# Kernel tuning notes

Hardware: AMD Instinct MI355X
Metric: run time of the kernel (lower is better)

The kernel has to match this reference:

```python
import jax, jax.numpy as jnp
import numpy as np

N = 4096          # num_nodes
D_MODEL = 256     # embedding_dim
H = 8             # num_heads
DH = D_MODEL // H # dim_head = 32
E_RAND = N * 32   # random edges (avg degree 32)


def setup_inputs() -> dict:
    key = jax.random.key(0)
    ks = jax.random.split(key, 12)
    s = 0.02
    x = jax.random.normal(ks[0], (N, D_MODEL), jnp.float32)
    src = jax.random.randint(ks[1], (E_RAND,), 0, N)
    dst = jax.random.randint(ks[2], (E_RAND,), 0, N)
    loops = jnp.arange(N)
    # add self-loops so no softmax row is all -inf
    edge_index = jnp.stack([jnp.concatenate([src, loops]),
                            jnp.concatenate([dst, loops])]).astype(jnp.int64)
    Wq = jax.random.normal(ks[3], (D_MODEL, D_MODEL), jnp.float32) * s
    bq = jnp.zeros((D_MODEL,), jnp.float32)
    Wk = jax.random.normal(ks[4], (D_MODEL, D_MODEL), jnp.float32) * s
    bk = jnp.zeros((D_MODEL,), jnp.float32)
    Wv = jax.random.normal(ks[5], (D_MODEL, D_MODEL), jnp.float32) * s
    bv = jnp.zeros((D_MODEL,), jnp.float32)
    Wp = jax.random.normal(ks[6], (D_MODEL, 2 * D_MODEL), jnp.float32) * s
    bp = jnp.zeros((D_MODEL,), jnp.float32)
    return {"x": x, "edge_index": edge_index,
            "Wq": Wq, "bq": bq, "Wk": Wk, "bk": bk,
            "Wv": Wv, "bv": bv, "Wp": Wp, "bp": bp}


def reference(x, edge_index, Wq, bq, Wk, bk, Wv, bv, Wp, bp):
    n = x.shape[0]
    # projections -> [H, N, DH]
    q = (x @ Wq.T + bq).reshape(n, H, DH).transpose(1, 0, 2)
    k = (x @ Wk.T + bk).reshape(n, H, DH).transpose(1, 0, 2)
    v = (x @ Wv.T + bv).reshape(n, H, DH).transpose(1, 0, 2)
    scale = 1.0 / jnp.sqrt(jnp.asarray(DH, x.dtype))
    att = jnp.einsum('hnd,hmd->hnm', q, k) * scale   # [H, N, N]
    # original: mask = ones(N,N); mask[e0,e1]=False; masked_fill(mask, -inf)
    allowed = jnp.zeros((n, n), bool).at[edge_index[0], edge_index[1]].set(True)
    att = jnp.where(allowed[None, :, :], att, -jnp.inf)
    att = jax.nn.softmax(att, axis=-1)
    y = jnp.einsum('hnm,hmd->hnd', att, v)            # [H, N, DH]
    y = y.transpose(1, 0, 2).reshape(n, H * DH)       # [N, D_MODEL]
    return jnp.concatenate([x, y], axis=1) @ Wp.T + bp
```

## Files before the change

kernel.cpp:

```cpp
#include <hip/hip_runtime.h>
#include <hip/hip_bf16.h>

typedef unsigned short u16;
typedef __attribute__((ext_vector_type(8))) short short8;
typedef __attribute__((ext_vector_type(4))) float f32x4;

#define MAXC 256

__device__ __forceinline__ float b2f(u16 b) {
    return __uint_as_float(((unsigned)b) << 16);
}
__device__ __forceinline__ u16 f2b(float f) {
    unsigned u = __float_as_uint(f);
    return (u16)((u + 0x7FFFu + ((u >> 16) & 1u)) >> 16);
}
__device__ __forceinline__ short8 load_cvt8(const float* __restrict__ p) {
    float4 f0 = *(const float4*)p;
    float4 f1 = *(const float4*)(p + 4);
    short8 r;
    r[0] = (short)f2b(f0.x); r[1] = (short)f2b(f0.y);
    r[2] = (short)f2b(f0.z); r[3] = (short)f2b(f0.w);
    r[4] = (short)f2b(f1.x); r[5] = (short)f2b(f1.y);
    r[6] = (short)f2b(f1.z); r[7] = (short)f2b(f1.w);
    return r;
}

__global__ __launch_bounds__(256) void prep_kernel(
    const int* __restrict__ e, int E,
    uint4* __restrict__ maskv, int mask16,
    unsigned* __restrict__ orbuf,
    const float* __restrict__ Wp, u16* __restrict__ wpb)
{
    int b = blockIdx.x, t = threadIdx.x;
    if (b < 192) {
        uint4 z = {0u, 0u, 0u, 0u};
        for (int i = b * 256 + t; i < mask16; i += 192 * 256) maskv[i] = z;
    } else if (b < 256) {
        int bb = b - 192;
        unsigned acc = 0;
        for (int i = bb * 256 + t; i < E; i += 64 * 256)
            acc |= (unsigned)e[2 * i + 1];
        __shared__ unsigned red[4];
        #pragma unroll
        for (int o = 32; o > 0; o >>= 1) acc |= __shfl_xor(acc, o, 64);
        if ((t & 63) == 0) red[t >> 6] = acc;
        __syncthreads();
        if (t == 0) orbuf[bb] = red[0] | red[1] | red[2] | red[3];
    } else {
        int i = (b - 256) * 256 + t;
        float4 f = ((const float4*)Wp)[i];
        u16* d = wpb + 4 * (size_t)i;
        d[0] = f2b(f.x); d[1] = f2b(f.y); d[2] = f2b(f.z); d[3] = f2b(f.w);
    }
}

__global__ __launch_bounds__(256) void scatter_qkv_kernel(
    const int* __restrict__ e, int E, int N,
    unsigned* __restrict__ mask, const unsigned* __restrict__ orbuf,
    const float* __restrict__ x,
    const float* __restrict__ Wq, const float* __restrict__ Wk,
    const float* __restrict__ Wv,
    const float* __restrict__ bq, const float* __restrict__ bk,
    const float* __restrict__ bv,
    u16* __restrict__ q, u16* __restrict__ k, u16* __restrict__ v)
{
    __shared__ u16 Wl[64][264];
    int t = threadIdx.x;

    if (blockIdx.x < 128) {
        unsigned oo = orbuf[t & 63];
        #pragma unroll
        for (int o = 32; o > 0; o >>= 1) oo |= __shfl_xor(oo, o, 64);
        bool i32mode = (oo != 0);
        int nw = N >> 5;
        for (int i = blockIdx.x * 256 + t; i < E; i += 128 * 256) {
            int row, col;
            if (i32mode) { row = e[i];     col = e[E + i]; }
            else         { row = e[2 * i]; col = e[2 * E + 2 * i]; }
            if ((unsigned)row < (unsigned)N && (unsigned)col < (unsigned)N)
                atomicOr(&mask[(size_t)row * nw + (col >> 5)], 1u << (col & 31));
        }
        return;
    }

    int bid = blockIdx.x - 128;
    int bx = bid & 31, by = bid >> 5;
    int which = by >> 2;
    int ncl = (by & 3) * 64;
    const float* Ws   = (which == 0) ? Wq : (which == 1) ? Wk : Wv;
    const float* bias = (which == 0) ? bq : (which == 1) ? bk : bv;
    u16*         T    = (which == 0) ? q  : (which == 1) ? k  : v;

    for (int s = t; s < 4096; s += 256) {
        int r  = s >> 6;
        int c4 = (s & 63) << 2;
        float4 f = *(const float4*)&Ws[(size_t)(ncl + r) * 256 + c4];
        Wl[r][c4 + 0] = f2b(f.x); Wl[r][c4 + 1] = f2b(f.y);
        Wl[r][c4 + 2] = f2b(f.z); Wl[r][c4 + 3] = f2b(f.w);
    }
    __syncthreads();

    int wv = t >> 6, l = t & 63, lr = l & 15, lk = l >> 4;
    int m0 = bx * 128 + wv * 32;
    f32x4 acc[2][4] = {};
    const float* a0b = x + (size_t)(m0 + lr) * 256 + lk * 8;
    const float* a1b = a0b + 16 * 256;

    #pragma unroll
    for (int kk = 0; kk < 8; kk++) {
        short8 a0 = load_cvt8(a0b + kk * 32);
        short8 a1 = load_cvt8(a1b + kk * 32);
        #pragma unroll
        for (int j = 0; j < 4; j++) {
            short8 b = *(const short8*)&Wl[j * 16 + lr][lk * 8 + kk * 32];
            acc[0][j] = __builtin_amdgcn_mfma_f32_16x16x32_bf16(a0, b, acc[0][j], 0, 0, 0);
            acc[1][j] = __builtin_amdgcn_mfma_f32_16x16x32_bf16(a1, b, acc[1][j], 0, 0, 0);
        }
    }
    #pragma unroll
    for (int i2 = 0; i2 < 2; i2++)
        #pragma unroll
        for (int j = 0; j < 4; j++)
            #pragma unroll
            for (int r = 0; r < 4; r++) {
                int grow = m0 + i2 * 16 + lk * 4 + r;
                int gc   = ncl + j * 16 + lr;
                T[(size_t)grow * 256 + gc] = f2b(acc[i2][j][r] + bias[gc]);
            }
}

__global__ __launch_bounds__(256) void attn_kernel(
    const unsigned* __restrict__ mask,
    const u16* __restrict__ qb, const u16* __restrict__ kb,
    const u16* __restrict__ vb, u16* __restrict__ yb, int N)
{
    __shared__ int   cols[4][MAXC];
    __shared__ float ws[4][8][16];
    __shared__ float fs[4][8];
    __shared__ float lsums[4][8];

    int t = threadIdx.x;
    int wv = t >> 6, lane = t & 63;
    int n = blockIdx.x * 4 + wv;
    int nw = N >> 5;

    unsigned wa = mask[(size_t)n * nw + lane];
    unsigned wb = mask[(size_t)n * nw + 64 + lane];
    int pc = __popc(wa) + __popc(wb);
    int scan = pc;
    #pragma unroll
    for (int o = 1; o < 64; o <<= 1) {
        int pv = __shfl_up(scan, o, 64);
        if (lane >= o) scan += pv;
    }
    int cnt = __shfl(scan, 63, 64);
    if (cnt > MAXC) cnt = MAXC;
    int off = scan - pc;
    while (wa && off < MAXC) {
        int b = __ffs(wa) - 1; wa &= wa - 1;
        cols[wv][off++] = (lane << 5) + b;
    }
    while (wb && off < MAXC) {
        int b = __ffs(wb) - 1; wb &= wb - 1;
        cols[wv][off++] = ((64 + lane) << 5) + b;
    }
    asm volatile("s_waitcnt lgkmcnt(0)" ::: "memory");

    int h8 = lane >> 4;
    int jl = lane & 15;
    int hv = lane >> 3;
    int d0 = lane * 4;

    const short8* qpA = (const short8*)(qb + (size_t)n * 256 + h8 * 32);
    const short8* qpB = (const short8*)(qb + (size_t)n * 256 + (h8 + 4) * 32);
    short8 qA0 = qpA[0], qA1 = qpA[1];
    short8 qB0 = qpB[0], qB1 = qpB[1];

    const float scale = 0.17677669529663687f;
    float mxA = -1e30f, mxB = -1e30f, lsA = 0.f, lsB = 0.f;
    float acc0 = 0.f, acc1 = 0.f, acc2 = 0.f, acc3 = 0.f;

    for (int c0 = 0; c0 < cnt; c0 += 16) {
        int cc = min(16, cnt - c0);
        float s0 = -1e30f, s1 = -1e30f;
        if (jl < cc) {
            const u16* kr = kb + (size_t)cols[wv][c0 + jl] * 256;
            short8 a0 = ((const short8*)(kr + h8 * 32))[0];
            short8 a1 = ((const short8*)(kr + h8 * 32))[1];
            short8 b0 = ((const short8*)(kr + (h8 + 4) * 32))[0];
            short8 b1 = ((const short8*)(kr + (h8 + 4) * 32))[1];
            float sa = 0.f, sb = 0.f;
            #pragma unroll
            for (int e2 = 0; e2 < 8; e2++) {
                sa = fmaf(b2f((u16)a0[e2]), b2f((u16)qA0[e2]), sa);
                sa = fmaf(b2f((u16)a1[e2]), b2f((u16)qA1[e2]), sa);
                sb = fmaf(b2f((u16)b0[e2]), b2f((u16)qB0[e2]), sb);
                sb = fmaf(b2f((u16)b1[e2]), b2f((u16)qB1[e2]), sb);
            }
            s0 = sa * scale; s1 = sb * scale;
        }
        float cm0 = s0, cm1 = s1;
        #pragma unroll
        for (int o = 8; o > 0; o >>= 1) {
            cm0 = fmaxf(cm0, __shfl_xor(cm0, o, 16));
            cm1 = fmaxf(cm1, __shfl_xor(cm1, o, 16));
        }
        float mnA = fmaxf(mxA, cm0), mnB = fmaxf(mxB, cm1);
        float fA = __expf(mxA - mnA), fB = __expf(mxB - mnB);
        float w0 = (jl < cc) ? __expf(s0 - mnA) : 0.f;
        float w1 = (jl < cc) ? __expf(s1 - mnB) : 0.f;
        float t0 = w0, t1 = w1;
        #pragma unroll
        for (int o = 8; o > 0; o >>= 1) {
            t0 += __shfl_xor(t0, o, 16);
            t1 += __shfl_xor(t1, o, 16);
        }
        lsA = lsA * fA + t0;  lsB = lsB * fB + t1;
        mxA = mnA;            mxB = mnB;

        ws[wv][h8][jl]     = w0;
        ws[wv][h8 + 4][jl] = w1;
        if (jl == 0) { fs[wv][h8] = fA; fs[wv][h8 + 4] = fB; }
        asm volatile("s_waitcnt lgkmcnt(0)" ::: "memory");

        float fv = fs[wv][hv];
        acc0 *= fv; acc1 *= fv; acc2 *= fv; acc3 *= fv;
        for (int j = 0; j < cc; j++) {
            float wj = ws[wv][hv][j];
            uint2 raw = *(const uint2*)(vb + (size_t)cols[wv][c0 + j] * 256 + d0);
            acc0 = fmaf(wj, b2f((u16)(raw.x & 0xffff)), acc0);
            acc1 = fmaf(wj, b2f((u16)(raw.x >> 16)),    acc1);
            acc2 = fmaf(wj, b2f((u16)(raw.y & 0xffff)), acc2);
            acc3 = fmaf(wj, b2f((u16)(raw.y >> 16)),    acc3);
        }
    }

    if (jl == 0) { lsums[wv][h8] = lsA; lsums[wv][h8 + 4] = lsB; }
    asm volatile("s_waitcnt lgkmcnt(0)" ::: "memory");
    float ls = lsums[wv][hv];
    uint2 ov;
    if (cnt > 0) {
        ov.x = (unsigned)f2b(acc0 / ls) | ((unsigned)f2b(acc1 / ls) << 16);
        ov.y = (unsigned)f2b(acc2 / ls) | ((unsigned)f2b(acc3 / ls) << 16);
    } else {
        ov.x = 0u; ov.y = 0u;
    }
    *(uint2*)(yb + (size_t)n * 256 + d0) = ov;
}

__global__ __launch_bounds__(256) void final_kernel(
    const float* __restrict__ x, const u16* __restrict__ yb,
    const u16* __restrict__ wpb, const float* __restrict__ bp,
    float* __restrict__ out)
{
    int t = threadIdx.x;
    int wv = t >> 6, l = t & 63, lr = l & 15, lk = l >> 4;
    int m0 = blockIdx.x * 64 + wv * 16;
    int n0 = blockIdx.y * 64;

    f32x4 acc[4] = {};
    const float* axb = x  + (size_t)(m0 + lr) * 256 + lk * 8;
    const u16*   ayb = yb + (size_t)(m0 + lr) * 256 + lk * 8;
    const short8* wp_ = (const short8*)(wpb + (size_t)(n0 + lr) * 512 + lk * 8);

    #pragma unroll
    for (int kk = 0; kk < 16; kk++) {
        short8 a;
        if (kk < 8) a = load_cvt8(axb + kk * 32);
        else        a = *(const short8*)(ayb + (kk - 8) * 32);
        #pragma unroll
        for (int j = 0; j < 4; j++) {
            short8 b = wp_[(size_t)j * 16 * 64 + kk * 4];
            acc[j] = __builtin_amdgcn_mfma_f32_16x16x32_bf16(a, b, acc[j], 0, 0, 0);
        }
    }
    #pragma unroll
    for (int j = 0; j < 4; j++)
        #pragma unroll
        for (int r = 0; r < 4; r++) {
            int grow = m0 + lk * 4 + r;
            int gc   = n0 + j * 16 + lr;
            out[(size_t)grow * 256 + gc] = acc[j][r] + bp[gc];
        }
}

extern "C" void kernel_launch(void* const* d_in, const int* in_sizes, int n_in,
                              void* d_out, int out_size, void* d_ws, size_t ws_size,
                              hipStream_t stream) {
    const float* x  = (const float*)d_in[0];
    const int*   ei = (const int*)d_in[1];
    const float* Wq = (const float*)d_in[2];
    const float* bq = (const float*)d_in[3];
    const float* Wk = (const float*)d_in[4];
    const float* bk = (const float*)d_in[5];
    const float* Wv = (const float*)d_in[6];
    const float* bv = (const float*)d_in[7];
    const float* Wp = (const float*)d_in[8];
    const float* bp = (const float*)d_in[9];
    float* out = (float*)d_out;

    const int D = 256;
    int N = in_sizes[0] / D;
    int E = in_sizes[1] / 2;

    size_t maskB = (size_t)N * (N >> 5) * sizeof(unsigned);
    char* ws = (char*)d_ws;
    unsigned* mask  = (unsigned*)ws;
    unsigned* orbuf = (unsigned*)(ws + maskB);
    u16* qbb = (u16*)(ws + maskB + 512);
    u16* kbb = qbb + (size_t)N * D;
    u16* vbb = kbb + (size_t)N * D;
    u16* ybb = vbb + (size_t)N * D;
    u16* wpb = ybb + (size_t)N * D;

    prep_kernel<<<384, 256, 0, stream>>>(ei, E, (uint4*)ws, (int)(maskB / 16),
                                         orbuf, Wp, wpb);

    scatter_qkv_kernel<<<512, 256, 0, stream>>>(
        ei, E, N, mask, orbuf, x, Wq, Wk, Wv, bq, bk, bv, qbb, kbb, vbb);

    attn_kernel<<<N / 4, 256, 0, stream>>>(mask, qbb, kbb, vbb, ybb, N);

    dim3 gf(N / 64, 4);
    final_kernel<<<gf, 256, 0, stream>>>(x, ybb, wpb, bp, out);
}
```

Before: 51.69 us.

## Fuse sparse attention with output projection via shared-memory y tile

```diff
diff --git a/kernel.cpp b/kernel.cpp
--- a/kernel.cpp
+++ b/kernel.cpp
@@ -129,19 +129,23 @@
             }
 }
 
-__global__ __launch_bounds__(256) void attn_kernel(
+__global__ __launch_bounds__(1024) void attn_final_kernel(
     const unsigned* __restrict__ mask,
     const u16* __restrict__ qb, const u16* __restrict__ kb,
-    const u16* __restrict__ vb, u16* __restrict__ yb, int N)
+    const u16* __restrict__ vb,
+    const float* __restrict__ x, const u16* __restrict__ wpb,
+    const float* __restrict__ bp, float* __restrict__ out, int N)
 {
-    __shared__ int   cols[4][MAXC];
-    __shared__ float ws[4][8][16];
-    __shared__ float fs[4][8];
-    __shared__ float lsums[4][8];
+    __shared__ int   cols[16][MAXC];
+    __shared__ float ws[16][8][16];
+    __shared__ float fs[16][8];
+    __shared__ float lsums[16][8];
+    __shared__ u16   ylds[16][264];
 
     int t = threadIdx.x;
     int wv = t >> 6, lane = t & 63;
-    int n = blockIdx.x * 4 + wv;
+    int m0 = blockIdx.x * 16;
+    int n = m0 + wv;
     int nw = N >> 5;
 
     unsigned wa = mask[(size_t)n * nw + lane];
@@ -237,51 +241,39 @@
 
     if (jl == 0) { lsums[wv][h8] = lsA; lsums[wv][h8 + 4] = lsB; }
     asm volatile("s_waitcnt lgkmcnt(0)" ::: "memory");
-    float ls = lsums[wv][hv];
+    float lsv = lsums[wv][hv];
     uint2 ov;
     if (cnt > 0) {
-        ov.x = (unsigned)f2b(acc0 / ls) | ((unsigned)f2b(acc1 / ls) << 16);
-        ov.y = (unsigned)f2b(acc2 / ls) | ((unsigned)f2b(acc3 / ls) << 16);
+        ov.x = (unsigned)f2b(acc0 / lsv) | ((unsigned)f2b(acc1 / lsv) << 16);
+        ov.y = (unsigned)f2b(acc2 / lsv) | ((unsigned)f2b(acc3 / lsv) << 16);
     } else {
         ov.x = 0u; ov.y = 0u;
     }
-    *(uint2*)(yb + (size_t)n * 256 + d0) = ov;
-}
-
-__global__ __launch_bounds__(256) void final_kernel(
-    const float* __restrict__ x, const u16* __restrict__ yb,
-    const u16* __restrict__ wpb, const float* __restrict__ bp,
-    float* __restrict__ out)
-{
-    int t = threadIdx.x;
-    int wv = t >> 6, l = t & 63, lr = l & 15, lk = l >> 4;
-    int m0 = blockIdx.x * 64 + wv * 16;
-    int n0 = blockIdx.y * 64;
-
-    f32x4 acc[4] = {};
-    const float* axb = x  + (size_t)(m0 + lr) * 256 + lk * 8;
-    const u16*   ayb = yb + (size_t)(m0 + lr) * 256 + lk * 8;
-    const short8* wp_ = (const short8*)(wpb + (size_t)(n0 + lr) * 512 + lk * 8);
-
-    #pragma unroll
-    for (int kk = 0; kk < 16; kk++) {
-        short8 a;
-        if (kk < 8) a = load_cvt8(axb + kk * 32);
-        else        a = *(const short8*)(ayb + (kk - 8) * 32);
-        #pragma unroll
-        for (int j = 0; j < 4; j++) {
-            short8 b = wp_[(size_t)j * 16 * 64 + kk * 4];
-            acc[j] = __builtin_amdgcn_mfma_f32_16x16x32_bf16(a, b, acc[j], 0, 0, 0);
-        }
-    }
-    #pragma unroll
-    for (int j = 0; j < 4; j++)
+    *(uint2*)&ylds[wv][d0] = ov;
+    __syncthreads();
+
+    {
+        int lr = lane & 15, lk = lane >> 4;
+        int n0 = wv * 16;
+        f32x4 facc = {};
+        const float* axb = x + (size_t)(m0 + lr) * 256 + lk * 8;
+        const short8* wp_ = (const short8*)(wpb + (size_t)(n0 + lr) * 512 + lk * 8);
+
+        #pragma unroll
+        for (int kk = 0; kk < 16; kk++) {
+            short8 a;
+            if (kk < 8) a = load_cvt8(axb + kk * 32);
+            else        a = *(const short8*)&ylds[lr][(kk - 8) * 32 + lk * 8];
+            short8 b = wp_[kk * 4];
+            facc = __builtin_amdgcn_mfma_f32_16x16x32_bf16(a, b, facc, 0, 0, 0);
+        }
         #pragma unroll
         for (int r = 0; r < 4; r++) {
             int grow = m0 + lk * 4 + r;
-            int gc   = n0 + j * 16 + lr;
-            out[(size_t)grow * 256 + gc] = acc[j][r] + bp[gc];
-        }
+            int gc   = n0 + lr;
+            out[(size_t)grow * 256 + gc] = facc[r] + bp[gc];
+        }
+    }
 }
 
 extern "C" void kernel_launch(void* const* d_in, const int* in_sizes, int n_in,
@@ -310,8 +302,7 @@
     u16* qbb = (u16*)(ws + maskB + 512);
     u16* kbb = qbb + (size_t)N * D;
     u16* vbb = kbb + (size_t)N * D;
-    u16* ybb = vbb + (size_t)N * D;
-    u16* wpb = ybb + (size_t)N * D;
+    u16* wpb = vbb + (size_t)N * D;
 
     prep_kernel<<<384, 256, 0, stream>>>(ei, E, (uint4*)ws, (int)(maskB / 16),
                                          orbuf, Wp, wpb);
@@ -319,8 +310,6 @@
     scatter_qkv_kernel<<<512, 256, 0, stream>>>(
         ei, E, N, mask, orbuf, x, Wq, Wk, Wv, bq, bk, bv, qbb, kbb, vbb);
 
-    attn_kernel<<<N / 4, 256, 0, stream>>>(mask, qbb, kbb, vbb, ybb, N);
-
-    dim3 gf(N / 64, 4);
-    final_kernel<<<gf, 256, 0, stream>>>(x, ybb, wpb, bp, out);
-}
+    attn_final_kernel<<<N / 16, 1024, 0, stream>>>(
+        mask, qbb, kbb, vbb, x, wpb, bp, out, N);
+}
```

Measured after the change: 54.72 us. +5.9%, slower.
